# Optimization experiments

Measured on AMD Instinct MI355X. Metric: run time of the kernel, lower is better.

Reference implementation:

```python
import jax, jax.numpy as jnp
import numpy as np

D_MODEL = 1024
N_HEADS = 16
D_K = D_MODEL // N_HEADS
RANK = 16
LORA_SCALING = 32.0 / RANK  # alpha / rank = 2.0
LN_EPS = 1e-5


def _lora_linear(x, w, b, A, B):
    # torch nn.Linear: x @ w.T + b ; LoRA: (x @ A @ B) * scaling
    return x @ w.T + b + (x @ A @ B) * LORA_SCALING


def setup_inputs() -> dict:
    key = jax.random.key(0)
    ks = jax.random.split(key, 20)
    d = {}
    d['x'] = jax.random.normal(ks[0], (4, 1024, D_MODEL), dtype=jnp.float32)
    i = 1
    for p in ('q', 'k', 'v', 'o'):
        d[f'{p}_w'] = jax.random.normal(ks[i], (D_MODEL, D_MODEL), dtype=jnp.float32) * (1.0 / np.sqrt(D_MODEL)); i += 1
        d[f'{p}_b'] = jax.random.normal(ks[i], (D_MODEL,), dtype=jnp.float32) * 0.01; i += 1
        d[f'{p}_A'] = jax.random.normal(ks[i], (D_MODEL, RANK), dtype=jnp.float32) * 0.01; i += 1
        d[f'{p}_B'] = jax.random.normal(ks[i], (RANK, D_MODEL), dtype=jnp.float32) * 0.01; i += 1
    d['ln_g'] = jnp.ones((D_MODEL,), dtype=jnp.float32)
    d['ln_b'] = jnp.zeros((D_MODEL,), dtype=jnp.float32)
    return d


def reference(x, q_w, q_b, q_A, q_B, k_w, k_b, k_A, k_B,
              v_w, v_b, v_A, v_B, o_w, o_b, o_A, o_B, ln_g, ln_b):
    B, S, _ = x.shape
    # QKV projections with LoRA, reshape to [B, H, S, d_k]
    def split_heads(t):
        return t.reshape(B, S, N_HEADS, D_K).transpose(0, 2, 1, 3)
    Q = split_heads(_lora_linear(x, q_w, q_b, q_A, q_B))
    K = split_heads(_lora_linear(x, k_w, k_b, k_A, k_B))
    V = split_heads(_lora_linear(x, v_w, v_b, v_A, v_B))

    scores = jnp.einsum('bhqd,bhkd->bhqk', Q, K) / jnp.sqrt(jnp.float32(D_K))
    attn = jax.nn.softmax(scores, axis=-1)  # dropout is identity in eval
    ctx = jnp.einsum('bhqk,bhkd->bhqd', attn, V)
    ctx = ctx.transpose(0, 2, 1, 3).reshape(B, S, D_MODEL)

    out = _lora_linear(ctx, o_w, o_b, o_A, o_B)
    # residual + LayerNorm
    h = out + x
    mu = jnp.mean(h, axis=-1, keepdims=True)
    var = jnp.mean(jnp.square(h - mu), axis=-1, keepdims=True)
    normed = (h - mu) * jax.lax.rsqrt(var + LN_EPS) * ln_g + ln_b
    return normed, attn.mean(axis=1)
```

## Files before the change

kernel.cpp:

```cpp
#include <hip/hip_runtime.h>

#define DMODEL 1024
#define NHEADS 16
#define DHEAD  64
#define RANK   16
#define BATCH  4
#define SEQ    1024
#define MTOT   (BATCH*SEQ)
#define QSCALE 0.18033688011112042f

typedef __bf16 bf16;
typedef __bf16 bf16x8 __attribute__((ext_vector_type(8)));
typedef __bf16 bf16x4 __attribute__((ext_vector_type(4)));
typedef float  f32x4  __attribute__((ext_vector_type(4)));

__device__ __forceinline__ int swz128(int row, int byte_in_row) {
  int slot = byte_in_row >> 4;
  return row * 128 + (((slot ^ (row & 7)) << 4) | (byte_in_row & 15));
}

__device__ __forceinline__ void gll16(const void* g, void* l) {
  __builtin_amdgcn_global_load_lds((const __attribute__((address_space(1))) unsigned int*)g,
                                   (__attribute__((address_space(3))) unsigned int*)l, 16, 0, 0);
}

#define TRRD(lo, hi, base, o0, o1)                                   \
  asm volatile("ds_read_b64_tr_b16 %0, %2 offset:" #o0 "\n\t"        \
               "ds_read_b64_tr_b16 %1, %2 offset:" #o1               \
               : "=v"(lo), "=v"(hi) : "v"(base));

__global__ void prep_kernel(
    const float* __restrict__ W0, const float* __restrict__ A0, const float* __restrict__ B0,
    const float* __restrict__ W1, const float* __restrict__ A1, const float* __restrict__ B1,
    const float* __restrict__ W2, const float* __restrict__ A2, const float* __restrict__ B2,
    const float* __restrict__ W3, const float* __restrict__ A3, const float* __restrict__ B3,
    bf16* __restrict__ out, const float* __restrict__ x, bf16* __restrict__ xb) {
  __shared__ float bsc[RANK];
  const int blk = blockIdx.x;
  if (blk < 4096) {
    const int l = blk >> 10;
    const float* W = l == 0 ? W0 : l == 1 ? W1 : l == 2 ? W2 : W3;
    const float* A = l == 0 ? A0 : l == 1 ? A1 : l == 2 ? A2 : A3;
    const float* Bm = l == 0 ? B0 : l == 1 ? B1 : l == 2 ? B2 : B3;
    bf16* o = out + (size_t)l * DMODEL * DMODEL;
    const int n = blk & 1023;
    if (threadIdx.x < RANK) bsc[threadIdx.x] = Bm[threadIdx.x * DMODEL + n] * 2.0f;
    __syncthreads();
    float br[RANK];
#pragma unroll
    for (int r = 0; r < RANK; ++r) br[r] = bsc[r];
    for (int k0 = 0; k0 < DMODEL; k0 += 256) {
      int k = k0 + threadIdx.x;
      float acc = W[n * DMODEL + k];
      const float4* arow = (const float4*)(A + k * RANK);
#pragma unroll
      for (int r4 = 0; r4 < 4; ++r4) {
        float4 a = arow[r4];
        acc += a.x*br[r4*4+0] + a.y*br[r4*4+1] + a.z*br[r4*4+2] + a.w*br[r4*4+3];
      }
      o[n * DMODEL + k] = (bf16)acc;
    }
  } else {
    int i = ((blk - 4096) * 256 + threadIdx.x) * 4;
    float4 v = *(const float4*)(x + i);
    bf16x4 o4 = { (bf16)v.x, (bf16)v.y, (bf16)v.z, (bf16)v.w };
    *(bf16x4*)(xb + i) = o4;
  }
}

__global__ __launch_bounds__(512) void gemm_qkv_kernel(
    const bf16* __restrict__ xb, const bf16* __restrict__ weff,
    const float* __restrict__ bq, const float* __restrict__ bk, const float* __restrict__ bv,
    bf16* __restrict__ Qb, bf16* __restrict__ Kb, bf16* __restrict__ Vb)
{
  __shared__ __align__(16) char sA[16384];
  __shared__ __align__(16) char sB[32768];
  const int tid = threadIdx.x, w = tid >> 6, lane = tid & 63;
  const int bid = blockIdx.x;
  const int nb = (bid & 7) * 48 + (bid >> 3);
  const int n0 = (nb % 12) * 256, m0 = (nb / 12) * 128;
  const int z = n0 >> 10;
  const float* bias = z == 0 ? bq : z == 1 ? bk : bv;
  bf16* outp = z == 0 ? Qb : (z == 1 ? Kb : Vb);
  const float scl = z == 0 ? QSCALE : 1.0f;
  const int wm = (w & 1) * 64, wn = (w >> 1) * 64;
  f32x4 acc[4][4] = {};

  const bf16* pA[2]; const bf16* pB[4]; char* lA[2]; char* lB[4];
#pragma unroll
  for (int i = 0; i < 2; ++i) {
    int ci = i * 8 + w;
    int row = ci * 8 + (lane >> 3);
    int ss = (lane & 7) ^ (row & 7);
    pA[i] = xb + (size_t)(m0 + row) * DMODEL + ss * 8;
    lA[i] = sA + ci * 1024;
  }
#pragma unroll
  for (int i = 0; i < 4; ++i) {
    int ci = i * 8 + w;
    int row = ci * 8 + (lane >> 3);
    int ss = (lane & 7) ^ (row & 7);
    pB[i] = weff + (size_t)(n0 + row) * DMODEL + ss * 8;
    lB[i] = sB + ci * 1024;
  }
  for (int kt = 0; kt < DMODEL / 64; ++kt) {
    const int kbase = kt * 64;
#pragma unroll
    for (int i = 0; i < 2; ++i) gll16(pA[i] + kbase, lA[i]);
#pragma unroll
    for (int i = 0; i < 4; ++i) gll16(pB[i] + kbase, lB[i]);
    __syncthreads();
#pragma unroll
    for (int ks = 0; ks < 2; ++ks) {
      bf16x8 af[4], bfg[4];
#pragma unroll
      for (int mi = 0; mi < 4; ++mi)
        af[mi] = *(const bf16x8*)(sA + swz128(wm + mi*16 + (lane & 15), ks*64 + (lane >> 4)*16));
#pragma unroll
      for (int ni = 0; ni < 4; ++ni)
        bfg[ni] = *(const bf16x8*)(sB + swz128(wn + ni*16 + (lane & 15), ks*64 + (lane >> 4)*16));
#pragma unroll
      for (int mi = 0; mi < 4; ++mi)
#pragma unroll
        for (int ni = 0; ni < 4; ++ni)
          acc[mi][ni] = __builtin_amdgcn_mfma_f32_16x16x32_bf16(af[mi], bfg[ni], acc[mi][ni], 0, 0, 0);
    }
    __syncthreads();
  }

#pragma unroll
  for (int mi = 0; mi < 4; ++mi) {
#pragma unroll
    for (int ni = 0; ni < 4; ++ni) {
      int col = n0 + wn + ni * 16 + (lane & 15);
      float bcol = bias[col & 1023];
      int h = (col >> 6) & 15, d = col & 63;
#pragma unroll
      for (int r = 0; r < 4; ++r) {
        int row = m0 + wm + mi * 16 + (lane >> 4) * 4 + r;
        float v = (acc[mi][ni][r] + bcol) * scl;
        int b = row >> 10, s = row & 1023;
        outp[(size_t)((b * NHEADS + h) * SEQ + s) * DHEAD + d] = (bf16)v;
      }
    }
  }
}

__global__ __launch_bounds__(512) void flash_kernel(
    const bf16* __restrict__ Qb, const bf16* __restrict__ Kb, const bf16* __restrict__ Vb,
    bf16* __restrict__ ctx, float* __restrict__ lstat)
{
  __shared__ __align__(16) char sK[2 * 8192];
  __shared__ __align__(16) char sV[2 * 8192];
  __shared__ __align__(16) char sP[8 * 2048];
  const int tid = threadIdx.x, w = tid >> 6, lane = tid & 63;
  const int bid = blockIdx.x;
  const int nb = (bid & 7) * 64 + (bid >> 3);
  const int bh = nb >> 3;
  const int q0 = (nb & 7) * 128;
  const bf16* Qbase = Qb + (size_t)bh * SEQ * DHEAD;
  const bf16* Kbase = Kb + (size_t)bh * SEQ * DHEAD;
  const bf16* Vbase = Vb + (size_t)bh * SEQ * DHEAD;
  const int qw = q0 + w * 16;

  bf16x8 aq[2];
#pragma unroll
  for (int ks = 0; ks < 2; ++ks)
    aq[ks] = *(const bf16x8*)(Qbase + (size_t)(qw + (lane & 15)) * DHEAD + ks * 32 + (lane >> 4) * 8);

  const bf16* pK; const bf16* pV; int lKo; int lVo;
  {
    int ci = w;
    int rowK = ci * 8 + (lane >> 3);
    int ssK = (lane & 7) ^ (rowK & 7);
    pK = Kbase + (size_t)rowK * DHEAD + ssK * 8;
    lKo = ci * 1024;
    int kV = ci * 8 + ((lane >> 5) & 1) * 4 + ((lane >> 1) & 3);
    int dV = (((lane >> 3) & 3) << 4) + ((lane & 1) << 3);
    pV = Vbase + (size_t)kV * DHEAD + dV;
    lVo = ci * 1024;
  }

  char* sPw = sP + w * 2048;
  const unsigned pbase = (unsigned)(uintptr_t)sPw + ((lane >> 4) << 8) + ((lane & 15) << 3);
  const unsigned vbase0 = (unsigned)(uintptr_t)sV + ((lane >> 4) << 10) + ((lane & 15) << 3);
  char* pwr = sPw + ((lane >> 4) << 3) + (lane & 15) * 32;

  f32x4 cacc[4] = {};
  float lsum[4] = {0.f, 0.f, 0.f, 0.f};

  gll16(pK, sK + lKo);
  gll16(pV, sV + lVo);
  __syncthreads();

  for (int kt = 0; kt < SEQ / 64; ++kt) {
    const int cur = (kt & 1) << 13, nxt = cur ^ 8192;
    if (kt + 1 < SEQ / 64) {
      const size_t kofs = (size_t)((kt + 1) * 64) * DHEAD;
      gll16(pK + kofs, sK + nxt + lKo);
      gll16(pV + kofs, sV + nxt + lVo);
    }

    f32x4 sc[4] = {};
    __builtin_amdgcn_s_setprio(1);
#pragma unroll
    for (int ks = 0; ks < 2; ++ks)
#pragma unroll
      for (int ni = 0; ni < 4; ++ni) {
        bf16x8 bk = *(const bf16x8*)(sK + cur + swz128(ni*16 + (lane & 15), ks*64 + (lane >> 4)*16));
        sc[ni] = __builtin_amdgcn_mfma_f32_16x16x32_bf16(aq[ks], bk, sc[ni], 0, 0, 0);
      }
    __builtin_amdgcn_s_setprio(0);

#pragma unroll
    for (int ni = 0; ni < 4; ++ni) {
      float p0 = __builtin_amdgcn_exp2f(sc[ni][0]);
      float p1 = __builtin_amdgcn_exp2f(sc[ni][1]);
      float p2 = __builtin_amdgcn_exp2f(sc[ni][2]);
      float p3 = __builtin_amdgcn_exp2f(sc[ni][3]);
      lsum[0] += p0; lsum[1] += p1; lsum[2] += p2; lsum[3] += p3;
      bf16x4 pb = { (bf16)p0, (bf16)p1, (bf16)p2, (bf16)p3 };
      *(bf16x4*)(pwr + ni * 512) = pb;
    }
    asm volatile("s_waitcnt lgkmcnt(0)" ::: "memory");

    unsigned long long t0, t1, v0[4], v1[4];
    const unsigned vb = vbase0 + cur;
    TRRD(t0, t1, pbase, 0, 128)
    TRRD(v0[0], v1[0], vb, 0, 512)
    TRRD(v0[1], v1[1], vb, 128, 640)
    TRRD(v0[2], v1[2], vb, 256, 768)
    TRRD(v0[3], v1[3], vb, 384, 896)
    asm volatile("s_waitcnt lgkmcnt(0)" ::: "memory");
    __builtin_amdgcn_sched_barrier(0);
    {
      union { unsigned long long u[2]; bf16x8 v; } pu, vu;
      pu.u[0] = t0; pu.u[1] = t1;
      __builtin_amdgcn_s_setprio(1);
#pragma unroll
      for (int ni = 0; ni < 4; ++ni) {
        vu.u[0] = v0[ni]; vu.u[1] = v1[ni];
        cacc[ni] = __builtin_amdgcn_mfma_f32_16x16x32_bf16(pu.v, vu.v, cacc[ni], 0, 0, 0);
      }
      __builtin_amdgcn_s_setprio(0);
    }
    TRRD(t0, t1, pbase, 1024, 1152)
    TRRD(v0[0], v1[0], vb, 4096, 4608)
    TRRD(v0[1], v1[1], vb, 4224, 4736)
    TRRD(v0[2], v1[2], vb, 4352, 4864)
    TRRD(v0[3], v1[3], vb, 4480, 4992)
    asm volatile("s_waitcnt lgkmcnt(0)" ::: "memory");
    __builtin_amdgcn_sched_barrier(0);
    {
      union { unsigned long long u[2]; bf16x8 v; } pu, vu;
      pu.u[0] = t0; pu.u[1] = t1;
      __builtin_amdgcn_s_setprio(1);
#pragma unroll
      for (int ni = 0; ni < 4; ++ni) {
        vu.u[0] = v0[ni]; vu.u[1] = v1[ni];
        cacc[ni] = __builtin_amdgcn_mfma_f32_16x16x32_bf16(pu.v, vu.v, cacc[ni], 0, 0, 0);
      }
      __builtin_amdgcn_s_setprio(0);
    }
    __syncthreads();
  }

#pragma unroll
  for (int r = 0; r < 4; ++r) {
#pragma unroll
    for (int off = 1; off < 16; off <<= 1) lsum[r] += __shfl_xor(lsum[r], off);
  }

  const int b = bh >> 4, hh = bh & 15;
#pragma unroll
  for (int r = 0; r < 4; ++r) {
    float inv = __builtin_amdgcn_rcpf(lsum[r]);
    int qrow = qw + (lane >> 4) * 4 + r;
#pragma unroll
    for (int ni = 0; ni < 4; ++ni) {
      int d = ni * 16 + (lane & 15);
      ctx[(size_t)(b * SEQ + qrow) * DMODEL + hh * DHEAD + d] = (bf16)(cacc[ni][r] * inv);
    }
    if ((lane & 15) == 0) lstat[(size_t)bh * SEQ + qrow] = lsum[r];
  }
}

__global__ __launch_bounds__(256) void tail_kernel(
    const bf16* __restrict__ Qb, const bf16* __restrict__ Kb,
    const float* __restrict__ lstat, float* __restrict__ out2,
    const bf16* __restrict__ ctx, const bf16* __restrict__ weffo,
    const float* __restrict__ bias, const float* __restrict__ resid,
    float* __restrict__ outf)
{
  __shared__ __align__(16) char smem[2 * 16384];
  const int tid = threadIdx.x, w = tid >> 6, lane = tid & 63;

  if (blockIdx.x < 512) {
    char* sK = smem;
    const int bid = blockIdx.x;
    const int nb2 = (bid & 7) * 64 + (bid >> 3);
    const int b = nb2 >> 7;
    const int q0 = ((nb2 >> 3) & 15) * 64, k0 = (nb2 & 7) * 128;
    const int qw = q0 + w * 16;
    size_t goff[4]; int lofs[4];
#pragma unroll
    for (int i = 0; i < 4; ++i) {
      int chunk = i * 4 + w;
      int row = chunk * 8 + (lane >> 3);
      int ss = (lane & 7) ^ (row & 7);
      goff[i] = (size_t)(k0 + row) * DHEAD + ss * 8;
      lofs[i] = chunk * 1024;
    }
    const bf16* Kb_b = Kb + (size_t)b * NHEADS * SEQ * DHEAD;
    const bf16* Qb_b = Qb + (size_t)b * NHEADS * SEQ * DHEAD;

    f32x4 macc[8] = {};
#pragma unroll
    for (int i = 0; i < 4; ++i) gll16(Kb_b + goff[i], sK + lofs[i]);
    asm volatile("s_waitcnt vmcnt(0)" ::: "memory");
    __syncthreads();

    for (int h = 0; h < NHEADS; ++h) {
      const int cur = (h & 1) << 14, nxt = cur ^ 16384;
      if (h + 1 < NHEADS) {
        const bf16* Kn = Kb_b + (size_t)(h + 1) * SEQ * DHEAD;
#pragma unroll
        for (int i = 0; i < 4; ++i) gll16(Kn + goff[i], sK + nxt + lofs[i]);
      }
      const bf16* Qbase = Qb_b + (size_t)h * SEQ * DHEAD;
      bf16x8 aq[2];
#pragma unroll
      for (int ks = 0; ks < 2; ++ks)
        aq[ks] = *(const bf16x8*)(Qbase + (size_t)(qw + (lane & 15)) * DHEAD
                                  + ks * 32 + (lane >> 4) * 8);
      char* cK = sK + cur;
      f32x4 sc[8] = {};
#pragma unroll
      for (int ks = 0; ks < 2; ++ks)
#pragma unroll
        for (int ni = 0; ni < 8; ++ni) {
          bf16x8 bk = *(const bf16x8*)(cK + swz128(ni*16 + (lane & 15), ks*64 + (lane >> 4)*16));
          sc[ni] = __builtin_amdgcn_mfma_f32_16x16x32_bf16(aq[ks], bk, sc[ni], 0, 0, 0);
        }
      float lsc[4];
      const float* ls = lstat + ((size_t)(b * NHEADS + h)) * SEQ;
#pragma unroll
      for (int r = 0; r < 4; ++r)
        lsc[r] = 0.0625f * __builtin_amdgcn_rcpf(ls[qw + (lane >> 4)*4 + r]);
#pragma unroll
      for (int ni = 0; ni < 8; ++ni)
#pragma unroll
        for (int r = 0; r < 4; ++r)
          macc[ni][r] += __builtin_amdgcn_exp2f(sc[ni][r]) * lsc[r];
      asm volatile("s_waitcnt vmcnt(0)" ::: "memory");
      __syncthreads();
    }
#pragma unroll
    for (int r = 0; r < 4; ++r) {
      int qrow = qw + (lane >> 4) * 4 + r;
#pragma unroll
      for (int ni = 0; ni < 8; ++ni)
        out2[(size_t)(b * SEQ + qrow) * SEQ + k0 + ni * 16 + (lane & 15)] = macc[ni][r];
    }
  } else {
    char* sA = smem; char* sB = smem + 8192;
    const int bid = blockIdx.x - 512;
    const int nb = (bid & 7) * 64 + (bid >> 3);
    const int n0 = (nb & 7) * 128, m0 = (nb >> 3) * 64;
    const int wm = (w & 1) * 32, wn = (w >> 1) * 64;
    f32x4 acc[2][4] = {};
    const bf16* pA[2]; char* lA[2];
    const bf16* pB[4]; char* lB[4];
#pragma unroll
    for (int i = 0; i < 2; ++i) {
      int chunk = i * 4 + w;
      int row = chunk * 8 + (lane >> 3);
      int ss = (lane & 7) ^ (row & 7);
      pA[i] = ctx + (size_t)(m0 + row) * DMODEL + ss * 8;
      lA[i] = sA + chunk * 1024;
    }
#pragma unroll
    for (int i = 0; i < 4; ++i) {
      int chunk = i * 4 + w;
      int row = chunk * 8 + (lane >> 3);
      int ss = (lane & 7) ^ (row & 7);
      pB[i] = weffo + (size_t)(n0 + row) * DMODEL + ss * 8;
      lB[i] = sB + chunk * 1024;
    }
    for (int kt = 0; kt < DMODEL / 64; ++kt) {
      const int kbase = kt * 64;
#pragma unroll
      for (int i = 0; i < 2; ++i) gll16(pA[i] + kbase, lA[i]);
#pragma unroll
      for (int i = 0; i < 4; ++i) gll16(pB[i] + kbase, lB[i]);
      __syncthreads();
#pragma unroll
      for (int ks = 0; ks < 2; ++ks) {
        bf16x8 af[2], bfg[4];
#pragma unroll
        for (int mi = 0; mi < 2; ++mi)
          af[mi] = *(const bf16x8*)(sA + swz128(wm + mi*16 + (lane & 15), ks*64 + (lane >> 4)*16));
#pragma unroll
        for (int ni = 0; ni < 4; ++ni)
          bfg[ni] = *(const bf16x8*)(sB + swz128(wn + ni*16 + (lane & 15), ks*64 + (lane >> 4)*16));
#pragma unroll
        for (int mi = 0; mi < 2; ++mi)
#pragma unroll
          for (int ni = 0; ni < 4; ++ni)
            acc[mi][ni] = __builtin_amdgcn_mfma_f32_16x16x32_bf16(af[mi], bfg[ni], acc[mi][ni], 0, 0, 0);
      }
      __syncthreads();
    }
#pragma unroll
    for (int mi = 0; mi < 2; ++mi) {
#pragma unroll
      for (int ni = 0; ni < 4; ++ni) {
        int col = n0 + wn + ni * 16 + (lane & 15);
        float bcol = bias[col];
#pragma unroll
        for (int r = 0; r < 4; ++r) {
          int row = m0 + wm + mi * 16 + (lane >> 4) * 4 + r;
          outf[(size_t)row * DMODEL + col] =
              acc[mi][ni][r] + bcol + resid[(size_t)row * DMODEL + col];
        }
      }
    }
  }
}

__global__ __launch_bounds__(256) void ln_kernel(
    float* __restrict__ hb, const float* __restrict__ g,
    const float* __restrict__ bvec, float* __restrict__ out)
{
  const int row = blockIdx.x, t = threadIdx.x;
  float4 v = *(const float4*)(hb + (size_t)row * DMODEL + t * 4);
  float s = v.x + v.y + v.z + v.w;
  float s2 = v.x*v.x + v.y*v.y + v.z*v.z + v.w*v.w;
#pragma unroll
  for (int off = 32; off >= 1; off >>= 1) {
    s  += __shfl_down(s, off);
    s2 += __shfl_down(s2, off);
  }
  __shared__ float red[8];
  const int w = t >> 6;
  if ((t & 63) == 0) { red[w] = s; red[4 + w] = s2; }
  __syncthreads();
  if (t == 0) {
    red[0] = red[0] + red[1] + red[2] + red[3];
    red[4] = red[4] + red[5] + red[6] + red[7];
  }
  __syncthreads();
  float mu = red[0] * (1.0f / DMODEL);
  float var = red[4] * (1.0f / DMODEL) - mu * mu;
  float rs = rsqrtf(var + 1e-5f);
  float4 gv = *(const float4*)(g + t * 4);
  float4 bv = *(const float4*)(bvec + t * 4);
  float4 o;
  o.x = (v.x - mu) * rs * gv.x + bv.x;
  o.y = (v.y - mu) * rs * gv.y + bv.y;
  o.z = (v.z - mu) * rs * gv.z + bv.z;
  o.w = (v.w - mu) * rs * gv.w + bv.w;
  *(float4*)(out + (size_t)row * DMODEL + t * 4) = o;
}

extern "C" void kernel_launch(void* const* d_in, const int* in_sizes, int n_in,
                              void* d_out, int out_size, void* d_ws, size_t ws_size,
                              hipStream_t stream) {
  (void)in_sizes; (void)n_in; (void)out_size; (void)ws_size;
  const float* x = (const float*)d_in[0];
  const float* w_[4]  = {(const float*)d_in[1],  (const float*)d_in[5],
                         (const float*)d_in[9],  (const float*)d_in[13]};
  const float* b_[4]  = {(const float*)d_in[2],  (const float*)d_in[6],
                         (const float*)d_in[10], (const float*)d_in[14]};
  const float* A_[4]  = {(const float*)d_in[3],  (const float*)d_in[7],
                         (const float*)d_in[11], (const float*)d_in[15]};
  const float* Bm_[4] = {(const float*)d_in[4],  (const float*)d_in[8],
                         (const float*)d_in[12], (const float*)d_in[16]};
  const float* lng = (const float*)d_in[17];
  const float* lnb = (const float*)d_in[18];

  char* ws = (char*)d_ws;
  bf16* xb    = (bf16*)(ws);
  bf16* weff  = (bf16*)(ws + (8u  << 20));
  bf16* Qb    = (bf16*)(ws + (16u << 20));
  bf16* Kb    = (bf16*)(ws + (24u << 20));
  bf16* Vb    = (bf16*)(ws + (32u << 20));
  float* lstat = (float*)(ws + (40u << 20));
  bf16* ctx = xb;
  float* hbuf = (float*)d_out;
  float* out2 = (float*)d_out + (size_t)MTOT * DMODEL;

  prep_kernel<<<dim3(8192), dim3(256), 0, stream>>>(
      w_[0], A_[0], Bm_[0], w_[1], A_[1], Bm_[1],
      w_[2], A_[2], Bm_[2], w_[3], A_[3], Bm_[3], weff, x, xb);

  gemm_qkv_kernel<<<dim3(384), 512, 0, stream>>>(
      xb, weff, b_[0], b_[1], b_[2], Qb, Kb, Vb);

  flash_kernel<<<dim3(512), 512, 0, stream>>>(Qb, Kb, Vb, ctx, lstat);

  tail_kernel<<<dim3(1024), 256, 0, stream>>>(
      Qb, Kb, lstat, out2,
      ctx, weff + 3u * DMODEL * DMODEL, b_[3], x, hbuf);

  ln_kernel<<<dim3(MTOT), 256, 0, stream>>>(hbuf, lng, lnb, hbuf);
}
```

Baseline: 122.4 us.

## Rewrite flash attention with 32x32 MFMA, register P via permlane swap, transposed V

```diff
diff --git a/kernel.cpp b/kernel.cpp
--- a/kernel.cpp
+++ b/kernel.cpp
@@ -13,6 +13,7 @@
 typedef __bf16 bf16x8 __attribute__((ext_vector_type(8)));
 typedef __bf16 bf16x4 __attribute__((ext_vector_type(4)));
 typedef float  f32x4  __attribute__((ext_vector_type(4)));
+typedef float  f32x16 __attribute__((ext_vector_type(16)));
 
 __device__ __forceinline__ int swz128(int row, int byte_in_row) {
   int slot = byte_in_row >> 4;
@@ -24,10 +25,13 @@
                                    (__attribute__((address_space(3))) unsigned int*)l, 16, 0, 0);
 }
 
-#define TRRD(lo, hi, base, o0, o1)                                   \
-  asm volatile("ds_read_b64_tr_b16 %0, %2 offset:" #o0 "\n\t"        \
-               "ds_read_b64_tr_b16 %1, %2 offset:" #o1               \
-               : "=v"(lo), "=v"(hi) : "v"(base));
+__device__ __forceinline__ unsigned pack2(float a, float b) {
+  union { bf16 h[2]; unsigned u; } x;
+  x.h[0] = (bf16)a; x.h[1] = (bf16)b;
+  return x.u;
+}
+
+#define PSWAP(a, b) asm volatile("v_permlane32_swap_b32 %0, %1" : "+v"(a), "+v"(b));
 
 __global__ void prep_kernel(
     const float* __restrict__ W0, const float* __restrict__ A0, const float* __restrict__ B0,
@@ -71,7 +75,7 @@
 __global__ __launch_bounds__(512) void gemm_qkv_kernel(
     const bf16* __restrict__ xb, const bf16* __restrict__ weff,
     const float* __restrict__ bq, const float* __restrict__ bk, const float* __restrict__ bv,
-    bf16* __restrict__ Qb, bf16* __restrict__ Kb, bf16* __restrict__ Vb)
+    bf16* __restrict__ Qb, bf16* __restrict__ Kb, bf16* __restrict__ Vt)
 {
   __shared__ __align__(16) char sA[16384];
   __shared__ __align__(16) char sB[32768];
@@ -81,7 +85,6 @@
   const int n0 = (nb % 12) * 256, m0 = (nb / 12) * 128;
   const int z = n0 >> 10;
   const float* bias = z == 0 ? bq : z == 1 ? bk : bv;
-  bf16* outp = z == 0 ? Qb : (z == 1 ? Kb : Vb);
   const float scl = z == 0 ? QSCALE : 1.0f;
   const int wm = (w & 1) * 64, wn = (w >> 1) * 64;
   f32x4 acc[4][4] = {};
@@ -128,161 +131,158 @@
     __syncthreads();
   }
 
-#pragma unroll
-  for (int mi = 0; mi < 4; ++mi) {
-#pragma unroll
-    for (int ni = 0; ni < 4; ++ni) {
-      int col = n0 + wn + ni * 16 + (lane & 15);
-      float bcol = bias[col & 1023];
-      int h = (col >> 6) & 15, d = col & 63;
-#pragma unroll
-      for (int r = 0; r < 4; ++r) {
-        int row = m0 + wm + mi * 16 + (lane >> 4) * 4 + r;
-        float v = (acc[mi][ni][r] + bcol) * scl;
-        int b = row >> 10, s = row & 1023;
-        outp[(size_t)((b * NHEADS + h) * SEQ + s) * DHEAD + d] = (bf16)v;
-      }
-    }
-  }
-}
-
-__global__ __launch_bounds__(512) void flash_kernel(
-    const bf16* __restrict__ Qb, const bf16* __restrict__ Kb, const bf16* __restrict__ Vb,
+  if (z < 2) {
+    bf16* outp = z == 0 ? Qb : Kb;
+#pragma unroll
+    for (int mi = 0; mi < 4; ++mi) {
+#pragma unroll
+      for (int ni = 0; ni < 4; ++ni) {
+        int col = n0 + wn + ni * 16 + (lane & 15);
+        float bcol = bias[col & 1023];
+        int h = (col >> 6) & 15, d = col & 63;
+#pragma unroll
+        for (int r = 0; r < 4; ++r) {
+          int row = m0 + wm + mi * 16 + (lane >> 4) * 4 + r;
+          float v = (acc[mi][ni][r] + bcol) * scl;
+          int b = row >> 10, s = row & 1023;
+          outp[(size_t)((b * NHEADS + h) * SEQ + s) * DHEAD + d] = (bf16)v;
+        }
+      }
+    }
+  } else {
+#pragma unroll
+    for (int mi = 0; mi < 4; ++mi) {
+#pragma unroll
+      for (int ni = 0; ni < 4; ++ni) {
+        int col = n0 + wn + ni * 16 + (lane & 15);
+        float bcol = bias[col & 1023];
+        int h = (col >> 6) & 15, d = col & 63;
+        int row0 = m0 + wm + mi * 16 + (lane >> 4) * 4;
+        int b = row0 >> 10, s = row0 & 1023;
+        bf16x4 pv;
+#pragma unroll
+        for (int r = 0; r < 4; ++r) pv[r] = (bf16)(acc[mi][ni][r] + bcol);
+        *(bf16x4*)(Vt + (size_t)((b * NHEADS + h) * DHEAD + d) * SEQ + s) = pv;
+      }
+    }
+  }
+}
+
+__global__ __launch_bounds__(256) void flash_kernel(
+    const bf16* __restrict__ Qb, const bf16* __restrict__ Kb, const bf16* __restrict__ Vt,
     bf16* __restrict__ ctx, float* __restrict__ lstat)
 {
   __shared__ __align__(16) char sK[2 * 8192];
   __shared__ __align__(16) char sV[2 * 8192];
-  __shared__ __align__(16) char sP[8 * 2048];
   const int tid = threadIdx.x, w = tid >> 6, lane = tid & 63;
+  const int l31 = lane & 31, lh = lane >> 5;
   const int bid = blockIdx.x;
   const int nb = (bid & 7) * 64 + (bid >> 3);
   const int bh = nb >> 3;
   const int q0 = (nb & 7) * 128;
   const bf16* Qbase = Qb + (size_t)bh * SEQ * DHEAD;
   const bf16* Kbase = Kb + (size_t)bh * SEQ * DHEAD;
-  const bf16* Vbase = Vb + (size_t)bh * SEQ * DHEAD;
-  const int qw = q0 + w * 16;
-
-  bf16x8 aq[2];
-#pragma unroll
-  for (int ks = 0; ks < 2; ++ks)
-    aq[ks] = *(const bf16x8*)(Qbase + (size_t)(qw + (lane & 15)) * DHEAD + ks * 32 + (lane >> 4) * 8);
-
-  const bf16* pK; const bf16* pV; int lKo; int lVo;
-  {
-    int ci = w;
-    int rowK = ci * 8 + (lane >> 3);
-    int ssK = (lane & 7) ^ (rowK & 7);
-    pK = Kbase + (size_t)rowK * DHEAD + ssK * 8;
-    lKo = ci * 1024;
-    int kV = ci * 8 + ((lane >> 5) & 1) * 4 + ((lane >> 1) & 3);
-    int dV = (((lane >> 3) & 3) << 4) + ((lane & 1) << 3);
-    pV = Vbase + (size_t)kV * DHEAD + dV;
-    lVo = ci * 1024;
-  }
-
-  char* sPw = sP + w * 2048;
-  const unsigned pbase = (unsigned)(uintptr_t)sPw + ((lane >> 4) << 8) + ((lane & 15) << 3);
-  const unsigned vbase0 = (unsigned)(uintptr_t)sV + ((lane >> 4) << 10) + ((lane & 15) << 3);
-  char* pwr = sPw + ((lane >> 4) << 3) + (lane & 15) * 32;
-
-  f32x4 cacc[4] = {};
-  float lsum[4] = {0.f, 0.f, 0.f, 0.f};
-
-  gll16(pK, sK + lKo);
-  gll16(pV, sV + lVo);
+  const bf16* Vbase = Vt + (size_t)bh * DHEAD * SEQ;
+  const int qw = q0 + w * 32;
+
+  bf16x8 aq[4];
+#pragma unroll
+  for (int kb = 0; kb < 4; ++kb)
+    aq[kb] = *(const bf16x8*)(Qbase + (size_t)(qw + l31) * DHEAD + kb * 16 + lh * 8);
+
+  const bf16* pK[2]; const bf16* pV[2]; int lKo[2], lVo[2];
+#pragma unroll
+  for (int i = 0; i < 2; ++i) {
+    int ci = i * 4 + w;
+    int row = ci * 8 + (lane >> 3);
+    int ss = (lane & 7) ^ (row & 7);
+    pK[i] = Kbase + (size_t)row * DHEAD + ss * 8;
+    lKo[i] = ci * 1024;
+    pV[i] = Vbase + (size_t)row * SEQ + ss * 8;
+    lVo[i] = ci * 1024;
+  }
+
+  f32x16 oacc[2] = {};
+  float lsum = 0.f;
+
+#pragma unroll
+  for (int i = 0; i < 2; ++i) {
+    gll16(pK[i], sK + lKo[i]);
+    gll16(pV[i], sV + lVo[i]);
+  }
   __syncthreads();
 
   for (int kt = 0; kt < SEQ / 64; ++kt) {
     const int cur = (kt & 1) << 13, nxt = cur ^ 8192;
     if (kt + 1 < SEQ / 64) {
-      const size_t kofs = (size_t)((kt + 1) * 64) * DHEAD;
-      gll16(pK + kofs, sK + nxt + lKo);
-      gll16(pV + kofs, sV + nxt + lVo);
-    }
-
-    f32x4 sc[4] = {};
+#pragma unroll
+      for (int i = 0; i < 2; ++i) {
+        gll16(pK[i] + (size_t)(kt + 1) * 64 * DHEAD, sK + nxt + lKo[i]);
+        gll16(pV[i] + (kt + 1) * 64, sV + nxt + lVo[i]);
+      }
+    }
+
+    f32x16 s[2] = {};
     __builtin_amdgcn_s_setprio(1);
 #pragma unroll
-    for (int ks = 0; ks < 2; ++ks)
-#pragma unroll
-      for (int ni = 0; ni < 4; ++ni) {
-        bf16x8 bk = *(const bf16x8*)(sK + cur + swz128(ni*16 + (lane & 15), ks*64 + (lane >> 4)*16));
-        sc[ni] = __builtin_amdgcn_mfma_f32_16x16x32_bf16(aq[ks], bk, sc[ni], 0, 0, 0);
+    for (int ksb = 0; ksb < 2; ++ksb)
+#pragma unroll
+      for (int kb = 0; kb < 4; ++kb) {
+        bf16x8 ak = *(const bf16x8*)(sK + cur + swz128(ksb*32 + l31, kb*32 + lh*16));
+        s[ksb] = __builtin_amdgcn_mfma_f32_32x32x16_bf16(ak, aq[kb], s[ksb], 0, 0, 0);
       }
     __builtin_amdgcn_s_setprio(0);
 
-#pragma unroll
-    for (int ni = 0; ni < 4; ++ni) {
-      float p0 = __builtin_amdgcn_exp2f(sc[ni][0]);
-      float p1 = __builtin_amdgcn_exp2f(sc[ni][1]);
-      float p2 = __builtin_amdgcn_exp2f(sc[ni][2]);
-      float p3 = __builtin_amdgcn_exp2f(sc[ni][3]);
-      lsum[0] += p0; lsum[1] += p1; lsum[2] += p2; lsum[3] += p3;
-      bf16x4 pb = { (bf16)p0, (bf16)p1, (bf16)p2, (bf16)p3 };
-      *(bf16x4*)(pwr + ni * 512) = pb;
-    }
-    asm volatile("s_waitcnt lgkmcnt(0)" ::: "memory");
-
-    unsigned long long t0, t1, v0[4], v1[4];
-    const unsigned vb = vbase0 + cur;
-    TRRD(t0, t1, pbase, 0, 128)
-    TRRD(v0[0], v1[0], vb, 0, 512)
-    TRRD(v0[1], v1[1], vb, 128, 640)
-    TRRD(v0[2], v1[2], vb, 256, 768)
-    TRRD(v0[3], v1[3], vb, 384, 896)
-    asm volatile("s_waitcnt lgkmcnt(0)" ::: "memory");
-    __builtin_amdgcn_sched_barrier(0);
-    {
-      union { unsigned long long u[2]; bf16x8 v; } pu, vu;
-      pu.u[0] = t0; pu.u[1] = t1;
-      __builtin_amdgcn_s_setprio(1);
-#pragma unroll
-      for (int ni = 0; ni < 4; ++ni) {
-        vu.u[0] = v0[ni]; vu.u[1] = v1[ni];
-        cacc[ni] = __builtin_amdgcn_mfma_f32_16x16x32_bf16(pu.v, vu.v, cacc[ni], 0, 0, 0);
-      }
-      __builtin_amdgcn_s_setprio(0);
-    }
-    TRRD(t0, t1, pbase, 1024, 1152)
-    TRRD(v0[0], v1[0], vb, 4096, 4608)
-    TRRD(v0[1], v1[1], vb, 4224, 4736)
-    TRRD(v0[2], v1[2], vb, 4352, 4864)
-    TRRD(v0[3], v1[3], vb, 4480, 4992)
-    asm volatile("s_waitcnt lgkmcnt(0)" ::: "memory");
-    __builtin_amdgcn_sched_barrier(0);
-    {
-      union { unsigned long long u[2]; bf16x8 v; } pu, vu;
-      pu.u[0] = t0; pu.u[1] = t1;
-      __builtin_amdgcn_s_setprio(1);
-#pragma unroll
-      for (int ni = 0; ni < 4; ++ni) {
-        vu.u[0] = v0[ni]; vu.u[1] = v1[ni];
-        cacc[ni] = __builtin_amdgcn_mfma_f32_16x16x32_bf16(pu.v, vu.v, cacc[ni], 0, 0, 0);
-      }
-      __builtin_amdgcn_s_setprio(0);
-    }
+    bf16x8 paf[4];
+#pragma unroll
+    for (int ksb = 0; ksb < 2; ++ksb) {
+      float p[16];
+#pragma unroll
+      for (int r = 0; r < 16; ++r) {
+        p[r] = __builtin_amdgcn_exp2f(s[ksb][r]);
+        lsum += p[r];
+      }
+      unsigned a0 = pack2(p[0], p[1]),   b0 = pack2(p[4], p[5]);
+      unsigned a1 = pack2(p[2], p[3]),   b1 = pack2(p[6], p[7]);
+      PSWAP(a0, b0) PSWAP(a1, b1)
+      unsigned c0 = pack2(p[8], p[9]),   d0 = pack2(p[12], p[13]);
+      unsigned c1 = pack2(p[10], p[11]), d1 = pack2(p[14], p[15]);
+      PSWAP(c0, d0) PSWAP(c1, d1)
+      union { unsigned u[4]; bf16x8 v; } A0, A1;
+      A0.u[0] = a0; A0.u[1] = a1; A0.u[2] = b0; A0.u[3] = b1;
+      A1.u[0] = c0; A1.u[1] = c1; A1.u[2] = d0; A1.u[3] = d1;
+      paf[ksb * 2 + 0] = A0.v;
+      paf[ksb * 2 + 1] = A1.v;
+    }
+
+    __builtin_amdgcn_s_setprio(1);
+#pragma unroll
+    for (int kbg = 0; kbg < 4; ++kbg)
+#pragma unroll
+      for (int db = 0; db < 2; ++db) {
+        bf16x8 bv = *(const bf16x8*)(sV + cur + swz128(db*32 + l31, kbg*32 + lh*16));
+        oacc[db] = __builtin_amdgcn_mfma_f32_32x32x16_bf16(paf[kbg], bv, oacc[db], 0, 0, 0);
+      }
+    __builtin_amdgcn_s_setprio(0);
+
     __syncthreads();
   }
 
-#pragma unroll
-  for (int r = 0; r < 4; ++r) {
-#pragma unroll
-    for (int off = 1; off < 16; off <<= 1) lsum[r] += __shfl_xor(lsum[r], off);
-  }
+  lsum += __shfl_xor(lsum, 32);
+  float inv = __builtin_amdgcn_rcpf(lsum);
 
   const int b = bh >> 4, hh = bh & 15;
 #pragma unroll
-  for (int r = 0; r < 4; ++r) {
-    float inv = __builtin_amdgcn_rcpf(lsum[r]);
-    int qrow = qw + (lane >> 4) * 4 + r;
-#pragma unroll
-    for (int ni = 0; ni < 4; ++ni) {
-      int d = ni * 16 + (lane & 15);
-      ctx[(size_t)(b * SEQ + qrow) * DMODEL + hh * DHEAD + d] = (bf16)(cacc[ni][r] * inv);
-    }
-    if ((lane & 15) == 0) lstat[(size_t)bh * SEQ + qrow] = lsum[r];
-  }
+  for (int r = 0; r < 16; ++r) {
+    int q_r = (r & 3) + 8 * (r >> 2) + 4 * lh;
+    float sc = __shfl(inv, q_r);
+    int row = qw + q_r;
+#pragma unroll
+    for (int db = 0; db < 2; ++db)
+      ctx[(size_t)(b * SEQ + row) * DMODEL + hh * DHEAD + db * 32 + l31] =
+          (bf16)(oacc[db][r] * sc);
+  }
+  if (lane < 32) lstat[(size_t)bh * SEQ + qw + lane] = lsum;
 }
 
 __global__ __launch_bounds__(256) void tail_kernel(
@@ -484,7 +484,7 @@
   bf16* weff  = (bf16*)(ws + (8u  << 20));
   bf16* Qb    = (bf16*)(ws + (16u << 20));
   bf16* Kb    = (bf16*)(ws + (24u << 20));
-  bf16* Vb    = (bf16*)(ws + (32u << 20));
+  bf16* Vt    = (bf16*)(ws + (32u << 20));
   float* lstat = (float*)(ws + (40u << 20));
   bf16* ctx = xb;
   float* hbuf = (float*)d_out;
@@ -495,9 +495,9 @@
       w_[2], A_[2], Bm_[2], w_[3], A_[3], Bm_[3], weff, x, xb);
 
   gemm_qkv_kernel<<<dim3(384), 512, 0, stream>>>(
-      xb, weff, b_[0], b_[1], b_[2], Qb, Kb, Vb);
-
-  flash_kernel<<<dim3(512), 512, 0, stream>>>(Qb, Kb, Vb, ctx, lstat);
+      xb, weff, b_[0], b_[1], b_[2], Qb, Kb, Vt);
+
+  flash_kernel<<<dim3(512), 256, 0, stream>>>(Qb, Kb, Vt, ctx, lstat);
 
   tail_kernel<<<dim3(1024), 256, 0, stream>>>(
       Qb, Kb, lstat, out2,
```

After: 124.4 us. No clear change (+1.6%).
